# Performance work log

Measured on AMD Instinct MI355X. Metric: run time of the kernel, lower is better.

The kernel has to match this reference:

```python
import jax, jax.numpy as jnp
import numpy as np

# Config mirroring the TF module: cross-attention path (one_on_rna == 2),
# use_attn_augument=1, aug_multiply=0, two_d_softm=1, two_d_softm_mul_row_count=1,
# reduce_level=20 (protok used for padding masks).
B, L, D, H = 4, 1024, 512, 8
DEPTH = D // H          # 64, matches the repeat(64) in padding_to_zeros
NEG = -1.0e9


def setup_inputs() -> dict:
    key = jax.random.key(0)
    ks = jax.random.split(key, 16)
    s = np.float32(1.0 / np.sqrt(D))  # glorot-ish scale
    q = jax.random.normal(ks[0], (B, L, D), jnp.float32)
    kv = jax.random.normal(ks[1], (B, L, D), jnp.float32)
    # protein tokens; 0 == padding (compared against 0.0 in the TF code)
    protok = jax.random.randint(ks[2], (B, L), 0, 21).astype(jnp.float32)
    statpot_hb = jax.random.uniform(ks[3], (B, L, L), dtype=jnp.float32)
    statpot_pi = jax.random.uniform(ks[4], (B, L, L), dtype=jnp.float32)
    # cross padding mask: 1.0 where the protein (query) position is padding
    pad = (protok == 0.0).astype(jnp.float32)            # [B, L]
    cross_mask = jnp.broadcast_to(pad[:, :, None], (B, L, L)).astype(jnp.float32)
    wq = jax.random.normal(ks[5], (D, D), jnp.float32) * s
    wk = jax.random.normal(ks[6], (D, D), jnp.float32) * s
    wv = jax.random.normal(ks[7], (D, D), jnp.float32) * s
    wo = jax.random.normal(ks[8], (D, D), jnp.float32) * s
    bq = jnp.zeros((D,), jnp.float32)
    bk = jnp.zeros((D,), jnp.float32)
    bv = jnp.zeros((D,), jnp.float32)
    bo = jnp.zeros((D,), jnp.float32)
    aug_weight_att = jnp.ones((1,), jnp.float32)
    aug_weight_aug = jnp.ones((1,), jnp.float32)
    return dict(q=q, kv=kv, protok=protok, statpot_hb=statpot_hb,
                statpot_pi=statpot_pi, cross_mask=cross_mask,
                wq=wq, bq=bq, wk=wk, bk=bk, wv=wv, bv=bv, wo=wo, bo=bo,
                aug_weight_att=aug_weight_att, aug_weight_aug=aug_weight_aug)


def _split_heads(x):
    # [B, L, D] -> [B, H, L, depth]
    return x.reshape(B, L, H, DEPTH).transpose(0, 2, 1, 3)


def reference(q, kv, protok, statpot_hb, statpot_pi, cross_mask,
              wq, bq, wk, bk, wv, bv, wo, bo, aug_weight_att, aug_weight_aug):
    # padding_to_zeros: zero features at padded protein positions
    pad_keep = (protok != 0.0).astype(q.dtype)[:, :, None]   # [B, L, 1]
    qp = (q @ wq + bq) * pad_keep   # query side is the protein (len == max_pro_len)
    k = kv @ wk + bk
    v = kv @ wv + bv
    qh, kh, vh = _split_heads(qp), _split_heads(k), _split_heads(v)

    # unscaled QK^T (original does NOT divide by sqrt(depth))
    logits = jnp.einsum('bhqd,bhkd->bhqk', qh, kh)           # [B,H,L,L]

    # statistical-potential augmentation (aug_multiply == 0 -> additive)
    table = jnp.stack([statpot_hb, statpot_pi], axis=1)      # [B,2,L,L]
    table = jnp.repeat(table, H // 2, axis=1)                # [B,H,L,L]
    logits = logits / jnp.max(logits)
    logits = aug_weight_att * logits
    table = aug_weight_aug * table
    table = table / jnp.max(table)
    logits = logits + table

    # additive large-negative mask, broadcast over heads
    logits = logits + cross_mask[:, None, :, :] * NEG

    # 2D softmax jointly over (query, key) axes
    attn = jax.nn.softmax(logits.reshape(B, H, L * L), axis=-1).reshape(B, H, L, L)

    # rescale by number of non-padded protein rows (two_d_softm_mul_row_count)
    mul = jnp.count_nonzero(protok, axis=1).astype(attn.dtype)[:, None, None, None]
    attn = attn * mul
    attn = attn / jnp.max(attn)

    # output = attn^T @ v : contracts the QUERY axis (as in the original matmul)
    out = jnp.einsum('bhqk,bhqd->bhkd', attn, vh)            # [B,H,L,depth]
    out = out.transpose(0, 2, 1, 3).reshape(B, L, D)
    out = out @ wo + bo
    out = out * pad_keep                                     # final padding zeroing
    return out
```

## Files before the change

### kernel.cpp

```cpp
#include <hip/hip_runtime.h>
#include <math.h>

#define BB 4
#define LL 1024
#define DD 512
#define HH 8
#define DEP 64
#define NEGV (-1.0e9f)

typedef __attribute__((ext_vector_type(8))) short bf16x8;
typedef __attribute__((ext_vector_type(4))) float f32x4;
typedef unsigned short u16;
typedef unsigned int u32;

#define S_GMAX 0
#define S_TMAX 1
#define S_TMIN 2
#define S_MUL  4
#define S_SUM  8
#define S_M    40
#define S_C    72
#define P_TMAX 128
#define P_TMIN 384
#define P_GMAX 640
#define SCAL_F 1152
#define PER_T  (BB*HH*LL*DEP)

__device__ inline u16 f2b(float x) {
  u32 u = __float_as_uint(x);
  return (u16)((u + 0x7FFFu + ((u >> 16) & 1u)) >> 16);
}
__device__ inline float b2f(u16 h) { return __uint_as_float(((u32)h) << 16); }

__device__ inline void atomicMaxF(float* addr, float val) {
  unsigned int* ua = (unsigned int*)addr;
  unsigned int old = *ua;
  while (__uint_as_float(old) < val) {
    unsigned int assumed = old;
    old = atomicCAS(ua, assumed, __float_as_uint(val));
    if (old == assumed) break;
  }
}

__global__ void k0_init(float* ws) {
  int t = threadIdx.x;
  if (t < 4)  ws[S_MUL + t] = 0.0f;
  if (t < 32) { ws[S_SUM + t] = 0.0f; ws[S_M + t] = -INFINITY; ws[S_C + t] = 0.0f; }
}

__global__ void k_count(const float* __restrict__ protok, float* ws) {
  int b = blockIdx.x;
  int cnt = 0;
  for (int l = threadIdx.x; l < LL; l += blockDim.x)
    cnt += (protok[b*LL + l] != 0.0f) ? 1 : 0;
  __shared__ int sh[4];
  int lane = threadIdx.x & 63, w = threadIdx.x >> 6;
  #pragma unroll
  for (int o = 32; o > 0; o >>= 1) cnt += __shfl_down(cnt, o);
  if (lane == 0) sh[w] = cnt;
  __syncthreads();
  if (threadIdx.x == 0) ws[S_MUL + b] = (float)(sh[0] + sh[1] + sh[2] + sh[3]);
}

__global__ __launch_bounds__(256) void k_tminmax(const float* __restrict__ hb,
                                                 const float* __restrict__ pi,
                                                 float* __restrict__ ws) {
  const int g = blockIdx.x*256 + threadIdx.x;
  float mx = -INFINITY, mn = INFINITY;
  #pragma unroll
  for (int rep = 0; rep < 4; ++rep) {
    float4 a[4], c[4];
    #pragma unroll
    for (int j = 0; j < 4; ++j) {
      size_t idx = (size_t)rep*262144 + (size_t)j*65536 + g;
      a[j] = ((const float4*)hb)[idx];
      c[j] = ((const float4*)pi)[idx];
    }
    #pragma unroll
    for (int j = 0; j < 4; ++j) {
      mx = fmaxf(mx, fmaxf(fmaxf(a[j].x, a[j].y), fmaxf(a[j].z, a[j].w)));
      mx = fmaxf(mx, fmaxf(fmaxf(c[j].x, c[j].y), fmaxf(c[j].z, c[j].w)));
      mn = fminf(mn, fminf(fminf(a[j].x, a[j].y), fminf(a[j].z, a[j].w)));
      mn = fminf(mn, fminf(fminf(c[j].x, c[j].y), fminf(c[j].z, c[j].w)));
    }
  }
  __shared__ float shx[4], shn[4];
  int lane = threadIdx.x & 63, w = threadIdx.x >> 6;
  #pragma unroll
  for (int o = 32; o > 0; o >>= 1) {
    mx = fmaxf(mx, __shfl_down(mx, o));
    mn = fminf(mn, __shfl_down(mn, o));
  }
  if (lane == 0) { shx[w] = mx; shn[w] = mn; }
  __syncthreads();
  if (threadIdx.x == 0) {
    ws[P_TMAX + blockIdx.x] = fmaxf(fmaxf(shx[0], shx[1]), fmaxf(shx[2], shx[3]));
    ws[P_TMIN + blockIdx.x] = fminf(fminf(shn[0], shn[1]), fminf(shn[2], shn[3]));
  }
}

__global__ void k_red(float* __restrict__ ws) {
  const int t = threadIdx.x;
  float gm = fmaxf(ws[P_GMAX + t], ws[P_GMAX + t + 256]);
  float tm = ws[P_TMAX + t];
  float tn = ws[P_TMIN + t];
  __shared__ float sg[4], st[4], sn[4];
  int lane = t & 63, w = t >> 6;
  #pragma unroll
  for (int o = 32; o > 0; o >>= 1) {
    gm = fmaxf(gm, __shfl_down(gm, o));
    tm = fmaxf(tm, __shfl_down(tm, o));
    tn = fminf(tn, __shfl_down(tn, o));
  }
  if (lane == 0) { sg[w] = gm; st[w] = tm; sn[w] = tn; }
  __syncthreads();
  if (t == 0) {
    ws[S_GMAX] = fmaxf(fmaxf(sg[0], sg[1]), fmaxf(sg[2], sg[3]));
    ws[S_TMAX] = fmaxf(fmaxf(st[0], st[1]), fmaxf(st[2], st[3]));
    ws[S_TMIN] = fminf(fminf(sn[0], sn[1]), fminf(sn[2], sn[3]));
  }
}

__global__ __launch_bounds__(256) void k_xb(const float* __restrict__ q,
                                            const float* __restrict__ kv,
                                            u16* __restrict__ Xb) {
  int tg = blockIdx.x*256 + threadIdx.x;
  int which = tg >> 18;
  size_t off8 = (size_t)(tg & 262143) * 8;
  const float* s = which ? kv : q;
  float4 f0 = *(const float4*)&s[off8];
  float4 f1 = *(const float4*)&s[off8 + 4];
  u32 p0 = (u32)f2b(f0.x) | ((u32)f2b(f0.y) << 16);
  u32 p1 = (u32)f2b(f0.z) | ((u32)f2b(f0.w) << 16);
  u32 p2 = (u32)f2b(f1.x) | ((u32)f2b(f1.y) << 16);
  u32 p3 = (u32)f2b(f1.z) | ((u32)f2b(f1.w) << 16);
  *(int4*)&Xb[(size_t)which*PER_T + off8] = make_int4(p0, p1, p2, p3);
}

__global__ __launch_bounds__(256) void k_wt(
    const float* __restrict__ wq, const float* __restrict__ wk,
    const float* __restrict__ wv, const float* __restrict__ wo,
    u16* __restrict__ WTb) {
  const int g = blockIdx.z;
  const float* W = (g==0)?wq:(g==1)?wk:(g==2)?wv:wo;
  const int k0 = blockIdx.x*64, n0 = blockIdx.y*64;
  __shared__ u16 Ls[64][72];
  const int t = threadIdx.x;
  {
    const int r = t>>2, c16 = (t&3)*16;
    float v[16];
    #pragma unroll
    for (int j=0;j<4;++j) {
      float4 f = *(const float4*)&W[(size_t)(k0+r)*DD + n0 + c16 + 4*j];
      v[4*j]=f.x; v[4*j+1]=f.y; v[4*j+2]=f.z; v[4*j+3]=f.w;
    }
    u32 pk_[8];
    #pragma unroll
    for (int j=0;j<8;++j) pk_[j] = (u32)f2b(v[2*j]) | ((u32)f2b(v[2*j+1])<<16);
    *(int4*)&Ls[r][c16]   = make_int4(pk_[0],pk_[1],pk_[2],pk_[3]);
    *(int4*)&Ls[r][c16+8] = make_int4(pk_[4],pk_[5],pk_[6],pk_[7]);
  }
  __syncthreads();
  {
    const int n = t>>2, kk = (t&3)*16;
    u16 u[16];
    #pragma unroll
    for (int j=0;j<16;++j) u[j] = Ls[kk+j][n];
    u32 q_[8];
    #pragma unroll
    for (int j=0;j<8;++j) q_[j] = (u32)u[2*j] | ((u32)u[2*j+1]<<16);
    size_t dst = ((size_t)(g*DD + n0 + n))*DD + k0 + kk;
    *(int4*)&WTb[dst]   = make_int4(q_[0],q_[1],q_[2],q_[3]);
    *(int4*)&WTb[dst+8] = make_int4(q_[4],q_[5],q_[6],q_[7]);
  }
}

__global__ __launch_bounds__(256) void k1_proj(
    const float* __restrict__ protok,
    const float* __restrict__ bq, const float* __restrict__ bk,
    const float* __restrict__ bv,
    const u16* __restrict__ Xb, const u16* __restrict__ WTb,
    u16* __restrict__ QPb, u16* __restrict__ KHb, u16* __restrict__ VTb) {
  const int gid = blockIdx.z;
  const u16* X = Xb + (gid == 0 ? 0 : (size_t)PER_T);
  const float* bia = (gid == 0) ? bq : (gid == 1) ? bk : bv;
  const int m0 = blockIdx.x*64;
  const int h  = blockIdx.y;
  __shared__ u16 As[64][72];
  __shared__ u16 Bs[64][72];
  const int t = threadIdx.x;
  const int w = t>>6, lane = t&63, i = lane&15, g2 = lane>>4;
  const int sr = t>>2, sc = (t&3)*16;

  f32x4 acc[4];
  #pragma unroll
  for (int ct=0;ct<4;++ct) acc[ct] = (f32x4){0.f,0.f,0.f,0.f};

  for (int kk0 = 0; kk0 < DD; kk0 += 64) {
    __syncthreads();
    {
      size_t sx = (size_t)(m0+sr)*DD + kk0 + sc;
      *(int4*)&As[sr][sc]   = *(const int4*)&X[sx];
      *(int4*)&As[sr][sc+8] = *(const int4*)&X[sx+8];
    }
    {
      size_t src = ((size_t)(gid*DD + h*64 + sr))*DD + kk0 + sc;
      *(int4*)&Bs[sr][sc]   = *(const int4*)&WTb[src];
      *(int4*)&Bs[sr][sc+8] = *(const int4*)&WTb[src+8];
    }
    __syncthreads();
    bf16x8 a0 = *(const bf16x8*)&As[16*w + i][g2*8];
    bf16x8 a1 = *(const bf16x8*)&As[16*w + i][32 + g2*8];
    #pragma unroll
    for (int ct=0; ct<4; ++ct) {
      bf16x8 b0 = *(const bf16x8*)&Bs[ct*16 + i][g2*8];
      bf16x8 b1 = *(const bf16x8*)&Bs[ct*16 + i][32 + g2*8];
      acc[ct] = __builtin_amdgcn_mfma_f32_16x16x32_bf16(a0, b0, acc[ct], 0,0,0);
      acc[ct] = __builtin_amdgcn_mfma_f32_16x16x32_bf16(a1, b1, acc[ct], 0,0,0);
    }
  }
  __syncthreads();
  const int lrow = 16*w + g2*4;
  if (gid == 2) {
    #pragma unroll
    for (int ct=0;ct<4;++ct)
      #pragma unroll
      for (int r=0;r<4;++r)
        As[lrow + r][ct*16 + i] = f2b(acc[ct][r] + bia[h*64 + ct*16 + i]);
    __syncthreads();
    const int b = m0 >> 10, l0 = m0 & 1023;
    const int d = t>>2, lc = (t&3)*16;
    u16 u[16];
    #pragma unroll
    for (int j=0;j<16;++j) u[j] = As[lc+j][d];
    u32 q_[8];
    #pragma unroll
    for (int j=0;j<8;++j) q_[j] = (u32)u[2*j] | ((u32)u[2*j+1]<<16);
    size_t dst = ((size_t)(b*HH + h)*DEP + d)*LL + l0 + lc;
    *(int4*)&VTb[dst]   = make_int4(q_[0],q_[1],q_[2],q_[3]);
    *(int4*)&VTb[dst+8] = make_int4(q_[4],q_[5],q_[6],q_[7]);
  } else {
    u16* Y = (gid == 0) ? QPb : KHb;
    #pragma unroll
    for (int ct=0;ct<4;++ct)
      #pragma unroll
      for (int r=0;r<4;++r) {
        int m = m0 + lrow + r;
        float keep = (gid == 0) ? ((protok[m] != 0.0f) ? 1.0f : 0.0f) : 1.0f;
        int b = m >> 10, l = m & 1023;
        float val = (acc[ct][r] + bia[h*64 + ct*16 + i]) * keep;
        Y[((size_t)(b*HH + h)*LL + l)*DEP + ct*16 + i] = f2b(val);
      }
  }
}

__global__ __launch_bounds__(256) void k3_gmax(
    const u16* __restrict__ QPb, const u16* __restrict__ KHb,
    float* __restrict__ wsf) {
  const int q0 = blockIdx.x*64, bh = blockIdx.y;
  __shared__ u16 Qs[64][72];
  __shared__ u16 Ks[2][64][72];
  const int t = threadIdx.x;
  const int w = t>>6, lane = t&63, i = lane&15, g2 = lane>>4;
  const int sr = t>>2, sc = (t&3)*16;
  const u16* Qb = QPb + (size_t)bh*LL*DEP;
  const u16* Kb = KHb + (size_t)bh*LL*DEP;
  {
    size_t sq = (size_t)(q0 + sr)*DEP + sc;
    *(int4*)&Qs[sr][sc]   = *(const int4*)&Qb[sq];
    *(int4*)&Qs[sr][sc+8] = *(const int4*)&Qb[sq+8];
  }
  int4 rn0 = *(const int4*)&Kb[(size_t)sr*DEP + sc];
  int4 rn1 = *(const int4*)&Kb[(size_t)sr*DEP + sc + 8];
  __syncthreads();
  *(int4*)&Ks[0][sr][sc]   = rn0;
  *(int4*)&Ks[0][sr][sc+8] = rn1;
  rn0 = *(const int4*)&Kb[(size_t)(64 + sr)*DEP + sc];
  rn1 = *(const int4*)&Kb[(size_t)(64 + sr)*DEP + sc + 8];
  __syncthreads();
  bf16x8 a0 = *(const bf16x8*)&Qs[16*w + i][g2*8];
  bf16x8 a1 = *(const bf16x8*)&Qs[16*w + i][32 + g2*8];
  float mx = -INFINITY;
  for (int kt = 0; kt < 16; ++kt) {
    const int cur = kt & 1;
    #pragma unroll
    for (int ct=0;ct<4;++ct) {
      bf16x8 b0 = *(const bf16x8*)&Ks[cur][ct*16 + i][g2*8];
      bf16x8 b1 = *(const bf16x8*)&Ks[cur][ct*16 + i][32 + g2*8];
      f32x4 z = (f32x4){0.f,0.f,0.f,0.f};
      z = __builtin_amdgcn_mfma_f32_16x16x32_bf16(a0, b0, z, 0,0,0);
      z = __builtin_amdgcn_mfma_f32_16x16x32_bf16(a1, b1, z, 0,0,0);
      mx = fmaxf(mx, fmaxf(fmaxf(z[0],z[1]), fmaxf(z[2],z[3])));
    }
    if (kt < 15) {
      __syncthreads();
      *(int4*)&Ks[cur^1][sr][sc]   = rn0;
      *(int4*)&Ks[cur^1][sr][sc+8] = rn1;
      if (kt < 14) {
        rn0 = *(const int4*)&Kb[(size_t)((kt+2)*64 + sr)*DEP + sc];
        rn1 = *(const int4*)&Kb[(size_t)((kt+2)*64 + sr)*DEP + sc + 8];
      }
      __syncthreads();
    }
  }
  __shared__ float red[4];
  #pragma unroll
  for (int o = 32; o > 0; o >>= 1) mx = fmaxf(mx, __shfl_down(mx, o));
  if (lane == 0) red[w] = mx;
  __syncthreads();
  if (t == 0)
    wsf[P_GMAX + bh*16 + blockIdx.x] = fmaxf(fmaxf(red[0],red[1]), fmaxf(red[2],red[3]));
}

__global__ __launch_bounds__(256) void k4_fused(
    const float* __restrict__ protok,
    const float* __restrict__ hb, const float* __restrict__ pi,
    const float* __restrict__ w_att, const float* __restrict__ w_aug,
    const u16* __restrict__ QPb, const u16* __restrict__ KHb,
    const u16* __restrict__ VTb, u16* __restrict__ Ob,
    float* __restrict__ wsf) {
  const int k0 = blockIdx.x*64;
  const int bh = blockIdx.y, b = bh>>3, h = bh&7;
  const float* tab = ((h < 4) ? hb : pi) + (size_t)b*LL*LL;
  const float gmax  = wsf[S_GMAX];
  const float tmaxr = wsf[S_TMAX], tminr = wsf[S_TMIN];
  const float wa = w_att[0], wg = w_aug[0];
  const float inv_g = wa / gmax;
  const float tden  = (wg >= 0.0f) ? (wg * tmaxr) : (wg * tminr);
  const float inv_t = wg / tden;

  __shared__ u16 Ks[64][72];
  __shared__ u16 Qs[64][72];
  __shared__ u16 Vt[64][72];
  __shared__ u16 Pt[64][72];
  const int t = threadIdx.x;
  const int w = t>>6, lane = t&63, i = lane&15, g2 = lane>>4;
  const int sr = t>>2, sc = (t&3)*16;
  const int qlb = 16*w + g2*4;

  {
    size_t sk = ((size_t)bh*LL + k0 + sr)*DEP + sc;
    *(int4*)&Ks[sr][sc]   = *(const int4*)&KHb[sk];
    *(int4*)&Ks[sr][sc+8] = *(const int4*)&KHb[sk+8];
  }
  int4 rq0 = *(const int4*)&QPb[((size_t)bh*LL + sr)*DEP + sc];
  int4 rq1 = *(const int4*)&QPb[((size_t)bh*LL + sr)*DEP + sc + 8];
  int4 rv0 = *(const int4*)&VTb[((size_t)bh*DEP + sr)*LL + sc];
  int4 rv1 = *(const int4*)&VTb[((size_t)bh*DEP + sr)*LL + sc + 8];
  float tvr[4][4];
  #pragma unroll
  for (int r=0;r<4;++r)
    #pragma unroll
    for (int ct=0;ct<4;++ct)
      tvr[r][ct] = tab[(size_t)(qlb + r)*LL + k0 + ct*16 + i];
  __syncthreads();
  bf16x8 kb0[4], kb1[4];
  #pragma unroll
  for (int ct=0;ct<4;++ct) {
    kb0[ct] = *(const bf16x8*)&Ks[ct*16 + i][g2*8];
    kb1[ct] = *(const bf16x8*)&Ks[ct*16 + i][32 + g2*8];
  }
  f32x4 accO[4];
  #pragma unroll
  for (int dt=0;dt<4;++dt) accO[dt] = (f32x4){0.f,0.f,0.f,0.f};
  float lsum = 0.0f, lmax = -INFINITY;

  for (int q0 = 0; q0 < LL; q0 += 64) {
    const bool more = (q0 + 64) < LL;
    __syncthreads();
    *(int4*)&Qs[sr][sc]   = rq0;
    *(int4*)&Qs[sr][sc+8] = rq1;
    *(int4*)&Vt[sr][sc]   = rv0;
    *(int4*)&Vt[sr][sc+8] = rv1;
    __syncthreads();
    if (more) {
      rq0 = *(const int4*)&QPb[((size_t)bh*LL + q0 + 64 + sr)*DEP + sc];
      rq1 = *(const int4*)&QPb[((size_t)bh*LL + q0 + 64 + sr)*DEP + sc + 8];
      rv0 = *(const int4*)&VTb[((size_t)bh*DEP + sr)*LL + q0 + 64 + sc];
      rv1 = *(const int4*)&VTb[((size_t)bh*DEP + sr)*LL + q0 + 64 + sc + 8];
    }
    bf16x8 a0 = *(const bf16x8*)&Qs[16*w + i][g2*8];
    bf16x8 a1 = *(const bf16x8*)&Qs[16*w + i][32 + g2*8];
    f32x4 s4[4];
    #pragma unroll
    for (int ct=0; ct<4; ++ct) {
      f32x4 z = (f32x4){0.f,0.f,0.f,0.f};
      z = __builtin_amdgcn_mfma_f32_16x16x32_bf16(a0, kb0[ct], z, 0,0,0);
      z = __builtin_amdgcn_mfma_f32_16x16x32_bf16(a1, kb1[ct], z, 0,0,0);
      s4[ct] = z;
    }
    float tv2[4][4];
    if (more) {
      #pragma unroll
      for (int r=0;r<4;++r)
        #pragma unroll
        for (int ct=0;ct<4;++ct)
          tv2[r][ct] = tab[(size_t)(q0 + 64 + qlb + r)*LL + k0 + ct*16 + i];
    }
    #pragma unroll
    for (int r=0;r<4;++r) {
      int qrow = q0 + qlb + r;
      float madd = (protok[b*LL + qrow] == 0.0f) ? NEGV : 0.0f;
      #pragma unroll
      for (int ct=0;ct<4;++ct) {
        float sp = s4[ct][r]*inv_g + tvr[r][ct]*inv_t + madd;
        lmax = fmaxf(lmax, sp);
        float p = __expf(sp);
        lsum += p;
        Pt[ct*16 + i][qlb + r] = f2b(p);
      }
    }
    __syncthreads();
    bf16x8 pa0 = *(const bf16x8*)&Pt[16*w + i][g2*8];
    bf16x8 pa1 = *(const bf16x8*)&Pt[16*w + i][32 + g2*8];
    #pragma unroll
    for (int dt=0; dt<4; ++dt) {
      bf16x8 v0 = *(const bf16x8*)&Vt[dt*16 + i][g2*8];
      bf16x8 v1 = *(const bf16x8*)&Vt[dt*16 + i][32 + g2*8];
      accO[dt] = __builtin_amdgcn_mfma_f32_16x16x32_bf16(pa0, v0, accO[dt], 0,0,0);
      accO[dt] = __builtin_amdgcn_mfma_f32_16x16x32_bf16(pa1, v1, accO[dt], 0,0,0);
    }
    if (more) {
      #pragma unroll
      for (int r=0;r<4;++r)
        #pragma unroll
        for (int ct=0;ct<4;++ct) tvr[r][ct] = tv2[r][ct];
    }
  }
  #pragma unroll
  for (int dt=0;dt<4;++dt)
    #pragma unroll
    for (int r=0;r<4;++r)
      Ob[((size_t)bh*LL + k0 + qlb + r)*DEP + dt*16 + i] = f2b(accO[dt][r]);
  __shared__ float rs[4], rm[4];
  #pragma unroll
  for (int o = 32; o > 0; o >>= 1) {
    lsum += __shfl_down(lsum, o);
    lmax = fmaxf(lmax, __shfl_down(lmax, o));
  }
  if (lane == 0) { rs[w] = lsum; rm[w] = lmax; }
  __syncthreads();
  if (t == 0) {
    atomicAdd(&wsf[S_SUM + bh], rs[0]+rs[1]+rs[2]+rs[3]);
    atomicMaxF(&wsf[S_M + bh], fmaxf(fmaxf(rm[0], rm[1]), fmaxf(rm[2], rm[3])));
  }
}

__global__ void k45_cbh(float* ws) {
  int t = threadIdx.x;
  __shared__ float a_sh[32];
  if (t < 32) {
    int b = t >> 3;
    float s = ws[S_SUM + t], m = ws[S_M + t], mul = ws[S_MUL + b];
    a_sh[t] = mul * __expf(m) / s;
  }
  __syncthreads();
  if (t < 32) {
    float amax = -INFINITY;
    #pragma unroll
    for (int i = 0; i < 32; ++i) amax = fmaxf(amax, a_sh[i]);
    int b = t >> 3;
    float s = ws[S_SUM + t], mul = ws[S_MUL + b];
    ws[S_C + t] = (mul / s) / amax;
  }
}

__global__ __launch_bounds__(256) void k5_out(
    const float* __restrict__ protok,
    const float* __restrict__ bo,
    const u16* __restrict__ WTb, const u16* __restrict__ Ob,
    const float* __restrict__ wsf, float* __restrict__ out) {
  const int m0 = blockIdx.x*64, n0 = blockIdx.y*64;
  const int b = m0 >> 10, l0 = m0 & 1023;
  __shared__ u16 As[64][72];
  __shared__ u16 Bs[64][72];
  const int t = threadIdx.x;
  const int w = t>>6, lane = t&63, i = lane&15, g2 = lane>>4;
  const int sr = t>>2, sc = (t&3)*16;
  f32x4 acc[4];
  #pragma unroll
  for (int ct=0;ct<4;++ct) acc[ct] = (f32x4){0.f,0.f,0.f,0.f};

  for (int kk0 = 0; kk0 < DD; kk0 += 64) {
    const int h = kk0 >> 6;
    const float cs = wsf[S_C + b*HH + h];
    __syncthreads();
    {
      union { int4 v[2]; u16 u[16]; } uu;
      size_t so = ((size_t)(b*HH + h)*LL + l0 + sr)*DEP + sc;
      uu.v[0] = *(const int4*)&Ob[so];
      uu.v[1] = *(const int4*)&Ob[so+8];
      u32 pk_[8];
      #pragma unroll
      for (int j=0;j<8;++j)
        pk_[j] = (u32)f2b(b2f(uu.u[2*j])*cs) | ((u32)f2b(b2f(uu.u[2*j+1])*cs)<<16);
      *(int4*)&As[sr][sc]   = make_int4(pk_[0],pk_[1],pk_[2],pk_[3]);
      *(int4*)&As[sr][sc+8] = make_int4(pk_[4],pk_[5],pk_[6],pk_[7]);
    }
    {
      size_t src = ((size_t)(3*DD + n0 + sr))*DD + kk0 + sc;
      *(int4*)&Bs[sr][sc]   = *(const int4*)&WTb[src];
      *(int4*)&Bs[sr][sc+8] = *(const int4*)&WTb[src+8];
    }
    __syncthreads();
    bf16x8 a0 = *(const bf16x8*)&As[16*w + i][g2*8];
    bf16x8 a1 = *(const bf16x8*)&As[16*w + i][32 + g2*8];
    #pragma unroll
    for (int ct=0; ct<4; ++ct) {
      bf16x8 b0 = *(const bf16x8*)&Bs[ct*16 + i][g2*8];
      bf16x8 b1 = *(const bf16x8*)&Bs[ct*16 + i][32 + g2*8];
      acc[ct] = __builtin_amdgcn_mfma_f32_16x16x32_bf16(a0, b0, acc[ct], 0,0,0);
      acc[ct] = __builtin_amdgcn_mfma_f32_16x16x32_bf16(a1, b1, acc[ct], 0,0,0);
    }
  }
  #pragma unroll
  for (int ct=0;ct<4;++ct)
    #pragma unroll
    for (int r=0;r<4;++r) {
      int m = m0 + 16*w + g2*4 + r;
      float keep = (protok[m] != 0.0f) ? 1.0f : 0.0f;
      out[(size_t)m*DD + n0 + ct*16 + i] = (acc[ct][r] + bo[n0 + ct*16 + i]) * keep;
    }
}

extern "C" void kernel_launch(void* const* d_in, const int* in_sizes, int n_in,
                              void* d_out, int out_size, void* d_ws, size_t ws_size,
                              hipStream_t stream) {
  const float* q      = (const float*)d_in[0];
  const float* kv     = (const float*)d_in[1];
  const float* protok = (const float*)d_in[2];
  const float* hb     = (const float*)d_in[3];
  const float* pi     = (const float*)d_in[4];
  const float* wq = (const float*)d_in[6];
  const float* bq = (const float*)d_in[7];
  const float* wk = (const float*)d_in[8];
  const float* bk = (const float*)d_in[9];
  const float* wv = (const float*)d_in[10];
  const float* bv = (const float*)d_in[11];
  const float* wo = (const float*)d_in[12];
  const float* bo = (const float*)d_in[13];
  const float* w_att = (const float*)d_in[14];
  const float* w_aug = (const float*)d_in[15];
  float* wsf = (float*)d_ws;
  float* out = (float*)d_out;

  u16* base = (u16*)(wsf + SCAL_F);
  u16* QPb = base;
  u16* KHb = QPb + PER_T;
  u16* VTb = KHb + PER_T;
  u16* Ob  = VTb + PER_T;
  u16* WTb = Ob  + PER_T;
  u16* Xb  = WTb + 4*DD*DD;

  k0_init   <<<1, 64, 0, stream>>>(wsf);
  k_count   <<<4, 256, 0, stream>>>(protok, wsf);
  k_tminmax <<<256, 256, 0, stream>>>(hb, pi, wsf);
  k_xb      <<<2048, 256, 0, stream>>>(q, kv, Xb);
  k_wt      <<<dim3(8, 8, 4), 256, 0, stream>>>(wq, wk, wv, wo, WTb);
  k1_proj   <<<dim3(64, 8, 3), 256, 0, stream>>>(protok, bq, bk, bv, Xb, WTb, QPb, KHb, VTb);
  k3_gmax   <<<dim3(16, 32), 256, 0, stream>>>(QPb, KHb, wsf);
  k_red     <<<1, 256, 0, stream>>>(wsf);
  k4_fused  <<<dim3(16, 32), 256, 0, stream>>>(protok, hb, pi, w_att, w_aug,
                                               QPb, KHb, VTb, Ob, wsf);
  k45_cbh   <<<1, 64, 0, stream>>>(wsf);
  k5_out    <<<dim3(64, 8), 256, 0, stream>>>(protok, bo, WTb, Ob, wsf, out);
}
```

Before: 211.5 us.

## Pre-transpose scaled bias table to bf16, split query axis across blocks

Adds a kernel that scales the statpot tables, converts them to bf16 and transposes them once, so the fused attention kernel reads contiguous bf16 vectors instead of strided fp32 scalars. Both the gmax kernel (4-way over keys) and the fused attention kernel (2-way over queries) are split to launch more blocks. The two partial outputs are summed in a new reduction kernel. This adds extra launches, a second output buffer and rounding of the bias table to bf16, which may perturb the softmax logits.

```diff
diff --git a/kernel.cpp b/kernel.cpp
--- a/kernel.cpp
+++ b/kernel.cpp
@@ -23,7 +23,7 @@
 #define P_TMAX 128
 #define P_TMIN 384
 #define P_GMAX 640
-#define SCAL_F 1152
+#define SCAL_F 2816
 #define PER_T  (BB*HH*LL*DEP)
 
 __device__ inline u16 f2b(float x) {
@@ -99,25 +99,79 @@
   }
 }
 
-__global__ void k_red(float* __restrict__ ws) {
-  const int t = threadIdx.x;
-  float gm = fmaxf(ws[P_GMAX + t], ws[P_GMAX + t + 256]);
+__global__ void k_red1(float* __restrict__ ws) {
+  const int t = threadIdx.x;
   float tm = ws[P_TMAX + t];
   float tn = ws[P_TMIN + t];
-  __shared__ float sg[4], st[4], sn[4];
+  __shared__ float st[4], sn[4];
   int lane = t & 63, w = t >> 6;
   #pragma unroll
   for (int o = 32; o > 0; o >>= 1) {
-    gm = fmaxf(gm, __shfl_down(gm, o));
     tm = fmaxf(tm, __shfl_down(tm, o));
     tn = fminf(tn, __shfl_down(tn, o));
   }
-  if (lane == 0) { sg[w] = gm; st[w] = tm; sn[w] = tn; }
+  if (lane == 0) { st[w] = tm; sn[w] = tn; }
   __syncthreads();
   if (t == 0) {
-    ws[S_GMAX] = fmaxf(fmaxf(sg[0], sg[1]), fmaxf(sg[2], sg[3]));
     ws[S_TMAX] = fmaxf(fmaxf(st[0], st[1]), fmaxf(st[2], st[3]));
     ws[S_TMIN] = fminf(fminf(sn[0], sn[1]), fminf(sn[2], sn[3]));
+  }
+}
+
+__global__ void k_red2(float* __restrict__ ws) {
+  const int t = threadIdx.x;
+  float gm = -INFINITY;
+  #pragma unroll
+  for (int j = 0; j < 8; ++j) gm = fmaxf(gm, ws[P_GMAX + j*256 + t]);
+  __shared__ float sg[4];
+  int lane = t & 63, w = t >> 6;
+  #pragma unroll
+  for (int o = 32; o > 0; o >>= 1) gm = fmaxf(gm, __shfl_down(gm, o));
+  if (lane == 0) sg[w] = gm;
+  __syncthreads();
+  if (t == 0) ws[S_GMAX] = fmaxf(fmaxf(sg[0], sg[1]), fmaxf(sg[2], sg[3]));
+}
+
+__global__ __launch_bounds__(256) void k_taug(
+    const float* __restrict__ hb, const float* __restrict__ pi,
+    const float* __restrict__ w_aug, const float* __restrict__ wsf,
+    u16* __restrict__ TG) {
+  const int z = blockIdx.z;
+  const int b = z >> 1, tb = z & 1;
+  const float wg = w_aug[0];
+  const float tmaxr = wsf[S_TMAX], tminr = wsf[S_TMIN];
+  const float tden = (wg >= 0.0f) ? (wg * tmaxr) : (wg * tminr);
+  const float sc_ = wg / tden;
+  const float* src = (tb ? pi : hb) + (size_t)b*LL*LL;
+  const int k0 = blockIdx.x*64, q0 = blockIdx.y*64;
+  __shared__ u16 Ls[64][72];
+  const int t = threadIdx.x;
+  {
+    const int r = t>>2, c16 = (t&3)*16;
+    float v[16];
+    #pragma unroll
+    for (int j=0;j<4;++j) {
+      float4 f = *(const float4*)&src[(size_t)(q0+r)*LL + k0 + c16 + 4*j];
+      v[4*j]=f.x*sc_; v[4*j+1]=f.y*sc_; v[4*j+2]=f.z*sc_; v[4*j+3]=f.w*sc_;
+    }
+    u32 pk_[8];
+    #pragma unroll
+    for (int j=0;j<8;++j) pk_[j] = (u32)f2b(v[2*j]) | ((u32)f2b(v[2*j+1])<<16);
+    *(int4*)&Ls[r][c16]   = make_int4(pk_[0],pk_[1],pk_[2],pk_[3]);
+    *(int4*)&Ls[r][c16+8] = make_int4(pk_[4],pk_[5],pk_[6],pk_[7]);
+  }
+  __syncthreads();
+  {
+    const int kk = t>>2, qc = (t&3)*16;
+    u16 u[16];
+    #pragma unroll
+    for (int j=0;j<16;++j) u[j] = Ls[qc+j][kk];
+    u32 q_[8];
+    #pragma unroll
+    for (int j=0;j<8;++j) q_[j] = (u32)u[2*j] | ((u32)u[2*j+1]<<16);
+    size_t dst = ((size_t)z*LL + k0 + kk)*LL + q0 + qc;
+    *(int4*)&TG[dst]   = make_int4(q_[0],q_[1],q_[2],q_[3]);
+    *(int4*)&TG[dst+8] = make_int4(q_[4],q_[5],q_[6],q_[7]);
   }
 }
 
@@ -257,7 +311,7 @@
 __global__ __launch_bounds__(256) void k3_gmax(
     const u16* __restrict__ QPb, const u16* __restrict__ KHb,
     float* __restrict__ wsf) {
-  const int q0 = blockIdx.x*64, bh = blockIdx.y;
+  const int q0 = blockIdx.x*64, bh = blockIdx.y, kz = blockIdx.z;
   __shared__ u16 Qs[64][72];
   __shared__ u16 Ks[2][64][72];
   const int t = threadIdx.x;
@@ -270,18 +324,19 @@
     *(int4*)&Qs[sr][sc]   = *(const int4*)&Qb[sq];
     *(int4*)&Qs[sr][sc+8] = *(const int4*)&Qb[sq+8];
   }
-  int4 rn0 = *(const int4*)&Kb[(size_t)sr*DEP + sc];
-  int4 rn1 = *(const int4*)&Kb[(size_t)sr*DEP + sc + 8];
+  const int kb = kz*4;
+  int4 rn0 = *(const int4*)&Kb[(size_t)(kb*64 + sr)*DEP + sc];
+  int4 rn1 = *(const int4*)&Kb[(size_t)(kb*64 + sr)*DEP + sc + 8];
   __syncthreads();
   *(int4*)&Ks[0][sr][sc]   = rn0;
   *(int4*)&Ks[0][sr][sc+8] = rn1;
-  rn0 = *(const int4*)&Kb[(size_t)(64 + sr)*DEP + sc];
-  rn1 = *(const int4*)&Kb[(size_t)(64 + sr)*DEP + sc + 8];
+  rn0 = *(const int4*)&Kb[(size_t)((kb+1)*64 + sr)*DEP + sc];
+  rn1 = *(const int4*)&Kb[(size_t)((kb+1)*64 + sr)*DEP + sc + 8];
   __syncthreads();
   bf16x8 a0 = *(const bf16x8*)&Qs[16*w + i][g2*8];
   bf16x8 a1 = *(const bf16x8*)&Qs[16*w + i][32 + g2*8];
   float mx = -INFINITY;
-  for (int kt = 0; kt < 16; ++kt) {
+  for (int kt = 0; kt < 4; ++kt) {
     const int cur = kt & 1;
     #pragma unroll
     for (int ct=0;ct<4;++ct) {
@@ -292,13 +347,13 @@
       z = __builtin_amdgcn_mfma_f32_16x16x32_bf16(a1, b1, z, 0,0,0);
       mx = fmaxf(mx, fmaxf(fmaxf(z[0],z[1]), fmaxf(z[2],z[3])));
     }
-    if (kt < 15) {
+    if (kt < 3) {
       __syncthreads();
       *(int4*)&Ks[cur^1][sr][sc]   = rn0;
       *(int4*)&Ks[cur^1][sr][sc+8] = rn1;
-      if (kt < 14) {
-        rn0 = *(const int4*)&Kb[(size_t)((kt+2)*64 + sr)*DEP + sc];
-        rn1 = *(const int4*)&Kb[(size_t)((kt+2)*64 + sr)*DEP + sc + 8];
+      if (kt < 2) {
+        rn0 = *(const int4*)&Kb[(size_t)((kb+kt+2)*64 + sr)*DEP + sc];
+        rn1 = *(const int4*)&Kb[(size_t)((kb+kt+2)*64 + sr)*DEP + sc + 8];
       }
       __syncthreads();
     }
@@ -309,25 +364,25 @@
   if (lane == 0) red[w] = mx;
   __syncthreads();
   if (t == 0)
-    wsf[P_GMAX + bh*16 + blockIdx.x] = fmaxf(fmaxf(red[0],red[1]), fmaxf(red[2],red[3]));
+    wsf[P_GMAX + (bh*16 + blockIdx.x)*4 + kz] =
+        fmaxf(fmaxf(red[0],red[1]), fmaxf(red[2],red[3]));
 }
 
 __global__ __launch_bounds__(256) void k4_fused(
     const float* __restrict__ protok,
-    const float* __restrict__ hb, const float* __restrict__ pi,
-    const float* __restrict__ w_att, const float* __restrict__ w_aug,
+    const u16* __restrict__ TG,
+    const float* __restrict__ w_att,
     const u16* __restrict__ QPb, const u16* __restrict__ KHb,
-    const u16* __restrict__ VTb, u16* __restrict__ Ob,
+    const u16* __restrict__ VTb,
+    u16* __restrict__ Ob0, u16* __restrict__ Ob1,
     float* __restrict__ wsf) {
   const int k0 = blockIdx.x*64;
   const int bh = blockIdx.y, b = bh>>3, h = bh&7;
-  const float* tab = ((h < 4) ? hb : pi) + (size_t)b*LL*LL;
-  const float gmax  = wsf[S_GMAX];
-  const float tmaxr = wsf[S_TMAX], tminr = wsf[S_TMIN];
-  const float wa = w_att[0], wg = w_aug[0];
-  const float inv_g = wa / gmax;
-  const float tden  = (wg >= 0.0f) ? (wg * tmaxr) : (wg * tminr);
-  const float inv_t = wg / tden;
+  const int qbase = blockIdx.z * 512;
+  u16* Obz = blockIdx.z ? Ob1 : Ob0;
+  const u16* tgp = TG + (size_t)(b*2 + ((h < 4) ? 0 : 1))*LL*LL;
+  const float gmax = wsf[S_GMAX];
+  const float inv_g = w_att[0] / gmax;
 
   __shared__ u16 Ks[64][72];
   __shared__ u16 Qs[64][72];
@@ -343,16 +398,14 @@
     *(int4*)&Ks[sr][sc]   = *(const int4*)&KHb[sk];
     *(int4*)&Ks[sr][sc+8] = *(const int4*)&KHb[sk+8];
   }
-  int4 rq0 = *(const int4*)&QPb[((size_t)bh*LL + sr)*DEP + sc];
-  int4 rq1 = *(const int4*)&QPb[((size_t)bh*LL + sr)*DEP + sc + 8];
-  int4 rv0 = *(const int4*)&VTb[((size_t)bh*DEP + sr)*LL + sc];
-  int4 rv1 = *(const int4*)&VTb[((size_t)bh*DEP + sr)*LL + sc + 8];
-  float tvr[4][4];
-  #pragma unroll
-  for (int r=0;r<4;++r)
-    #pragma unroll
-    for (int ct=0;ct<4;++ct)
-      tvr[r][ct] = tab[(size_t)(qlb + r)*LL + k0 + ct*16 + i];
+  int4 rq0 = *(const int4*)&QPb[((size_t)bh*LL + qbase + sr)*DEP + sc];
+  int4 rq1 = *(const int4*)&QPb[((size_t)bh*LL + qbase + sr)*DEP + sc + 8];
+  int4 rv0 = *(const int4*)&VTb[((size_t)bh*DEP + sr)*LL + qbase + sc];
+  int4 rv1 = *(const int4*)&VTb[((size_t)bh*DEP + sr)*LL + qbase + sc + 8];
+  uint2 tq[4];
+  #pragma unroll
+  for (int ct=0;ct<4;++ct)
+    tq[ct] = *(const uint2*)&tgp[(size_t)(k0 + ct*16 + i)*LL + qbase + qlb];
   __syncthreads();
   bf16x8 kb0[4], kb1[4];
   #pragma unroll
@@ -365,8 +418,8 @@
   for (int dt=0;dt<4;++dt) accO[dt] = (f32x4){0.f,0.f,0.f,0.f};
   float lsum = 0.0f, lmax = -INFINITY;
 
-  for (int q0 = 0; q0 < LL; q0 += 64) {
-    const bool more = (q0 + 64) < LL;
+  for (int q0 = qbase; q0 < qbase + 512; q0 += 64) {
+    const bool more = (q0 + 64) < (qbase + 512);
     __syncthreads();
     *(int4*)&Qs[sr][sc]   = rq0;
     *(int4*)&Qs[sr][sc+8] = rq1;
@@ -389,26 +442,35 @@
       z = __builtin_amdgcn_mfma_f32_16x16x32_bf16(a1, kb1[ct], z, 0,0,0);
       s4[ct] = z;
     }
-    float tv2[4][4];
+    uint2 tq2[4];
     if (more) {
       #pragma unroll
-      for (int r=0;r<4;++r)
-        #pragma unroll
-        for (int ct=0;ct<4;++ct)
-          tv2[r][ct] = tab[(size_t)(q0 + 64 + qlb + r)*LL + k0 + ct*16 + i];
-    }
-    #pragma unroll
-    for (int r=0;r<4;++r) {
-      int qrow = q0 + qlb + r;
-      float madd = (protok[b*LL + qrow] == 0.0f) ? NEGV : 0.0f;
+      for (int ct=0;ct<4;++ct)
+        tq2[ct] = *(const uint2*)&tgp[(size_t)(k0 + ct*16 + i)*LL + q0 + 64 + qlb];
+    }
+    float madd[4];
+    #pragma unroll
+    for (int r=0;r<4;++r)
+      madd[r] = (protok[b*LL + q0 + qlb + r] == 0.0f) ? NEGV : 0.0f;
+    #pragma unroll
+    for (int ct=0;ct<4;++ct) {
+      float tvv[4];
+      tvv[0] = b2f((u16)(tq[ct].x & 0xffffu));
+      tvv[1] = b2f((u16)(tq[ct].x >> 16));
+      tvv[2] = b2f((u16)(tq[ct].y & 0xffffu));
+      tvv[3] = b2f((u16)(tq[ct].y >> 16));
+      float pr[4];
       #pragma unroll
-      for (int ct=0;ct<4;++ct) {
-        float sp = s4[ct][r]*inv_g + tvr[r][ct]*inv_t + madd;
+      for (int r=0;r<4;++r) {
+        float sp = fmaf(s4[ct][r], inv_g, tvv[r] + madd[r]);
         lmax = fmaxf(lmax, sp);
         float p = __expf(sp);
         lsum += p;
-        Pt[ct*16 + i][qlb + r] = f2b(p);
+        pr[r] = p;
       }
+      u32 pk0 = (u32)f2b(pr[0]) | ((u32)f2b(pr[1])<<16);
+      u32 pk1 = (u32)f2b(pr[2]) | ((u32)f2b(pr[3])<<16);
+      *(uint2*)&Pt[ct*16 + i][qlb] = make_uint2(pk0, pk1);
     }
     __syncthreads();
     bf16x8 pa0 = *(const bf16x8*)&Pt[16*w + i][g2*8];
@@ -422,16 +484,14 @@
     }
     if (more) {
       #pragma unroll
-      for (int r=0;r<4;++r)
-        #pragma unroll
-        for (int ct=0;ct<4;++ct) tvr[r][ct] = tv2[r][ct];
+      for (int ct=0;ct<4;++ct) tq[ct] = tq2[ct];
     }
   }
   #pragma unroll
   for (int dt=0;dt<4;++dt)
     #pragma unroll
     for (int r=0;r<4;++r)
-      Ob[((size_t)bh*LL + k0 + qlb + r)*DEP + dt*16 + i] = f2b(accO[dt][r]);
+      Obz[((size_t)bh*LL + k0 + qlb + r)*DEP + dt*16 + i] = f2b(accO[dt][r]);
   __shared__ float rs[4], rm[4];
   #pragma unroll
   for (int o = 32; o > 0; o >>= 1) {
@@ -444,6 +504,23 @@
     atomicAdd(&wsf[S_SUM + bh], rs[0]+rs[1]+rs[2]+rs[3]);
     atomicMaxF(&wsf[S_M + bh], fmaxf(fmaxf(rm[0], rm[1]), fmaxf(rm[2], rm[3])));
   }
+}
+
+__global__ __launch_bounds__(256) void k_osum(const u16* __restrict__ O0,
+                                              const u16* __restrict__ O1,
+                                              u16* __restrict__ Od) {
+  size_t idx = ((size_t)blockIdx.x*256 + threadIdx.x) * 8;
+  uint4 x = *(const uint4*)&O0[idx];
+  uint4 y = *(const uint4*)&O1[idx];
+  uint4 o;
+  u32* xp = (u32*)&x; u32* yp = (u32*)&y; u32* op = (u32*)&o;
+  #pragma unroll
+  for (int j=0;j<4;++j) {
+    float lo = b2f((u16)(xp[j] & 0xffffu)) + b2f((u16)(yp[j] & 0xffffu));
+    float hi = b2f((u16)(xp[j] >> 16))     + b2f((u16)(yp[j] >> 16));
+    op[j] = (u32)f2b(lo) | ((u32)f2b(hi) << 16);
+  }
+  *(uint4*)&Od[idx] = o;
 }
 
 __global__ void k45_cbh(float* ws) {
@@ -548,20 +625,27 @@
   u16* QPb = base;
   u16* KHb = QPb + PER_T;
   u16* VTb = KHb + PER_T;
-  u16* Ob  = VTb + PER_T;
-  u16* WTb = Ob  + PER_T;
-  u16* Xb  = WTb + 4*DD*DD;
+  u16* XO  = VTb + PER_T;
+  u16* WTb = XO  + 2*PER_T;
+  u16* TG  = WTb + 4*DD*DD;
+  u16* Xb  = XO;
+  u16* Ob0 = XO;
+  u16* Ob1 = XO + PER_T;
+  u16* Obf = QPb;
 
   k0_init   <<<1, 64, 0, stream>>>(wsf);
   k_count   <<<4, 256, 0, stream>>>(protok, wsf);
   k_tminmax <<<256, 256, 0, stream>>>(hb, pi, wsf);
+  k_red1    <<<1, 256, 0, stream>>>(wsf);
+  k_taug    <<<dim3(16, 16, 8), 256, 0, stream>>>(hb, pi, w_aug, wsf, TG);
   k_xb      <<<2048, 256, 0, stream>>>(q, kv, Xb);
   k_wt      <<<dim3(8, 8, 4), 256, 0, stream>>>(wq, wk, wv, wo, WTb);
   k1_proj   <<<dim3(64, 8, 3), 256, 0, stream>>>(protok, bq, bk, bv, Xb, WTb, QPb, KHb, VTb);
-  k3_gmax   <<<dim3(16, 32), 256, 0, stream>>>(QPb, KHb, wsf);
-  k_red     <<<1, 256, 0, stream>>>(wsf);
-  k4_fused  <<<dim3(16, 32), 256, 0, stream>>>(protok, hb, pi, w_att, w_aug,
-                                               QPb, KHb, VTb, Ob, wsf);
+  k3_gmax   <<<dim3(16, 32, 4), 256, 0, stream>>>(QPb, KHb, wsf);
+  k_red2    <<<1, 256, 0, stream>>>(wsf);
+  k4_fused  <<<dim3(16, 32, 2), 256, 0, stream>>>(protok, TG, w_att,
+                                                  QPb, KHb, VTb, Ob0, Ob1, wsf);
+  k_osum    <<<1024, 256, 0, stream>>>(Ob0, Ob1, Obf);
   k45_cbh   <<<1, 64, 0, stream>>>(wsf);
-  k5_out    <<<dim3(64, 8), 256, 0, stream>>>(protok, bo, WTb, Ob, wsf, out);
-}
+  k5_out    <<<dim3(64, 8), 256, 0, stream>>>(protok, bo, WTb, Obf, wsf, out);
+}
```

After: 250.8 us. +18.6%, slower.
